# Performance work log

Hardware: AMD Instinct MI355X
Metric: run time of the kernel (lower is better)

## Reference

```python
import jax, jax.numpy as jnp
import numpy as np

B, G, T = 4096, 100, 24


def _greedy_dispatch(demand, caps, prices, slack_price):
    """Exact LP solution of: min prices@alloc + slack_price*slack
    s.t. 0<=alloc<=caps, sum(alloc)+slack = demand (per b,t).
    demand: [B,T] (nonneg), caps: [B,G,T], prices: [G], slack_price: scalar.
    Returns alloc [B,G,T], slack [B,T].
    """
    prices_all = jnp.concatenate([prices, slack_price[None]])        # [G+1]
    # slack capacity = demand itself (slack alone can absorb everything)
    caps_all = jnp.concatenate([caps, demand[:, None, :]], axis=1)    # [B,G+1,T]
    order = jnp.argsort(prices_all)                                   # merit order
    caps_s = caps_all[:, order, :]
    before = jnp.cumsum(caps_s, axis=1) - caps_s                      # capacity ahead in merit order
    alloc_s = jnp.clip(demand[:, None, :] - before, 0.0, caps_s)
    inv = jnp.argsort(order)
    alloc = alloc_s[:, inv, :]
    return alloc[:, :-1, :], alloc[:, -1, :]


def setup_inputs() -> dict:
    key = jax.random.key(0)
    k1, k2, k3, k4 = jax.random.split(key, 4)
    R_up = jax.random.uniform(k1, (B, G, T), dtype=jnp.float32)
    R_dn = jax.random.uniform(k2, (B, G, T), dtype=jnp.float32)
    omega_true = jax.random.normal(k3, (B, T), dtype=jnp.float32) * 5.0
    b_G = 10.0 + 40.0 * jax.random.uniform(k4, (G,), dtype=jnp.float32)  # marginal costs $/MWh
    return {
        "R_up": R_up,
        "R_dn": R_dn,
        "omega_true": omega_true,
        "b_G": b_G,
        "voll": jnp.float32(1000.0),
        "vosp": jnp.float32(500.0),
        "rt_up_ratio": jnp.float32(1.5),
        "rt_dn_ratio": jnp.float32(1.2),
    }


def reference(R_up, R_dn, omega_true, b_G, voll, vosp, rt_up_ratio, rt_dn_ratio):
    c_up = rt_up_ratio * b_G                                          # [G]
    c_dn = rt_dn_ratio * b_G                                          # [G]
    dem_up = jnp.maximum(omega_true, 0.0)                             # [B,T]
    dem_dn = jnp.maximum(-omega_true, 0.0)
    du, LS = _greedy_dispatch(dem_up, R_up, c_up, voll)
    dd, SP = _greedy_dispatch(dem_dn, R_dn, c_dn, vosp)
    rt_obj = (jnp.einsum('g,bgt->b', c_up, du)
              + jnp.einsum('g,bgt->b', c_dn, dd)
              + voll * LS.sum(axis=1) + vosp * SP.sum(axis=1))        # [B]
    return du, dd, LS, SP, rt_obj
```

## Files before the change

kernel.cpp:

```cpp
#include <hip/hip_runtime.h>

#define G_ 100
#define T_ 24
#define GP1 101
#define TILE (G_ * T_)
#define VPB (TILE / 4)
#define BLOCK 256
#define WPB 4

typedef float vfloat4 __attribute__((ext_vector_type(4)));

__global__ void setup_sort_kernel(const float* __restrict__ b_G,
                                  const float* __restrict__ voll,
                                  const float* __restrict__ vosp,
                                  const float* __restrict__ ru,
                                  const float* __restrict__ rd,
                                  int* __restrict__ order_out,
                                  float* __restrict__ price_out)
{
    __shared__ float pu[GP1], pd[GP1];
    int i = threadIdx.x;
    if (i < GP1) {
        if (i < G_) { float bg = b_G[i]; pu[i] = ru[0] * bg; pd[i] = rd[0] * bg; }
        else        { pu[i] = voll[0];   pd[i] = vosp[0]; }
    }
    __syncthreads();
    if (i < GP1) {
        float mu = pu[i], md = pd[i];
        int r0 = 0, r1 = 0;
        for (int j = 0; j < GP1; ++j) {
            float vu = pu[j], vd = pd[j];
            r0 += (vu < mu) || (vu == mu && j < i);
            r1 += (vd < md) || (vd == md && j < i);
        }
        order_out[r0] = i;        price_out[r0] = mu;
        order_out[GP1 + r1] = i;  price_out[GP1 + r1] = md;
    }
}

template<int N>
__device__ __forceinline__ void scan_chunk(int k0,
    float* __restrict__ tile, const int* __restrict__ ordp,
    const float* __restrict__ prp, float dem,
    float& before, float& objp, float& slackv)
{
    int gg[N]; float pr[N], cap[N];
#pragma unroll
    for (int j = 0; j < N; ++j) { gg[j] = ordp[k0 + j]; pr[j] = prp[k0 + j]; }
#pragma unroll
    for (int j = 0; j < N; ++j) {
        int gl = (gg[j] < G_) ? gg[j] : 0;
        cap[j] = tile[gl * T_];
    }
#pragma unroll
    for (int j = 0; j < N; ++j) {
        float c = (gg[j] == G_) ? dem : cap[j];
        float a = fminf(fmaxf(dem - before, 0.f), c);
        before += c;
        objp = fmaf(pr[j], a, objp);
        if (gg[j] == G_) slackv = a;
        else             tile[gg[j] * T_] = a;
    }
}

__global__ __launch_bounds__(BLOCK, 4) void dispatch_kernel(
    const float* __restrict__ R_up, const float* __restrict__ R_dn,
    const float* __restrict__ omega,
    const int* __restrict__ ord_ws, const float* __restrict__ pr_ws,
    float* __restrict__ out, int B)
{
    __shared__ float s_tile[WPB * TILE];
    __shared__ float s_obj[WPB];

    const int tid  = threadIdx.x;
    const int w    = tid >> 6;
    const int lane = tid & 63;
    const int b = __builtin_amdgcn_readfirstlane((blockIdx.x * WPB + w) >> 1);
    const int p = __builtin_amdgcn_readfirstlane(w & 1);

    const size_t bgt = (size_t)B * TILE;

    const vfloat4* __restrict__ src =
        (const vfloat4*)(p ? R_dn : R_up) + (size_t)b * VPB;
    vfloat4 buf[10];
#pragma unroll
    for (int j = 0; j < 9; ++j) buf[j] = src[lane + j * 64];
    if (lane < VPB - 576) buf[9] = src[lane + 576];

    float* __restrict__ tw = &s_tile[w * TILE];
#pragma unroll
    for (int j = 0; j < 9; ++j) *(vfloat4*)&tw[(lane + j * 64) * 4] = buf[j];
    if (lane < VPB - 576)       *(vfloat4*)&tw[(lane + 576) * 4]    = buf[9];
    __syncthreads();

    float objp = 0.f;
    if (lane < T_) {
        const float om  = omega[(size_t)b * T_ + lane];
        const float dem = p ? fmaxf(-om, 0.f) : fmaxf(om, 0.f);
        float* __restrict__ tile = tw + lane;
        const int*   __restrict__ ordp = ord_ws + p * GP1;
        const float* __restrict__ prp  = pr_ws  + p * GP1;
        float before = 0.f, slackv = 0.f;
        scan_chunk<16>( 0, tile, ordp, prp, dem, before, objp, slackv);
        scan_chunk<16>(16, tile, ordp, prp, dem, before, objp, slackv);
        scan_chunk<16>(32, tile, ordp, prp, dem, before, objp, slackv);
        scan_chunk<16>(48, tile, ordp, prp, dem, before, objp, slackv);
        scan_chunk<16>(64, tile, ordp, prp, dem, before, objp, slackv);
        scan_chunk<16>(80, tile, ordp, prp, dem, before, objp, slackv);
        scan_chunk< 5>(96, tile, ordp, prp, dem, before, objp, slackv);
        out[2 * bgt + (size_t)p * B * T_ + (size_t)b * T_ + lane] = slackv;
    }

#pragma unroll
    for (int off = 32; off; off >>= 1) objp += __shfl_xor(objp, off, 64);
    if (lane == 0) s_obj[w] = objp;
    __syncthreads();
    if (tid == 0)
        out[2 * bgt + 2 * (size_t)B * T_ + 2 * blockIdx.x]     = s_obj[0] + s_obj[1];
    if (tid == 64)
        out[2 * bgt + 2 * (size_t)B * T_ + 2 * blockIdx.x + 1] = s_obj[2] + s_obj[3];

    vfloat4* __restrict__ dst = (vfloat4*)out + ((size_t)p * B + b) * VPB;
#pragma unroll
    for (int j = 0; j < 9; ++j)
        dst[lane + j * 64] = *(const vfloat4*)&tw[(lane + j * 64) * 4];
    if (lane < VPB - 576)
        dst[lane + 576] = *(const vfloat4*)&tw[(lane + 576) * 4];
}

extern "C" void kernel_launch(void* const* d_in, const int* in_sizes, int n_in,
                              void* d_out, int out_size, void* d_ws, size_t ws_size,
                              hipStream_t stream)
{
    const float* R_up  = (const float*)d_in[0];
    const float* R_dn  = (const float*)d_in[1];
    const float* omega = (const float*)d_in[2];
    const float* b_G   = (const float*)d_in[3];
    const float* voll  = (const float*)d_in[4];
    const float* vosp  = (const float*)d_in[5];
    const float* ru    = (const float*)d_in[6];
    const float* rd    = (const float*)d_in[7];

    const int B = in_sizes[0] / TILE;
    float* out = (float*)d_out;

    int*   ord_ws = (int*)d_ws;
    float* pr_ws  = (float*)((char*)d_ws + 2 * GP1 * sizeof(int));

    setup_sort_kernel<<<1, 128, 0, stream>>>(b_G, voll, vosp, ru, rd, ord_ws, pr_ws);

    dispatch_kernel<<<(2 * B) / WPB, BLOCK, 0, stream>>>(
        R_up, R_dn, omega, ord_ws, pr_ws, out, B);
}
```

Measured before the change: 166.5 us.

## Process both up and down dispatch per wave with prefetch of down tile

Each wave now handles one batch element for both up and down directions instead of one direction, halving the grid. The R_dn tile is loaded into registers while the up scan runs, overlapping global loads with the LDS scan. Per-wave objective summation replaces the shared-memory cross-wave reduction and block-wide syncs, so only wave barriers remain. This halves the parallelism across waves and makes each wave's work serial across the two passes.

After: 172.5 us. 3.6% more time.

```diff
diff --git a/kernel.cpp b/kernel.cpp
--- a/kernel.cpp
+++ b/kernel.cpp
@@ -70,62 +70,74 @@
     float* __restrict__ out, int B)
 {
     __shared__ float s_tile[WPB * TILE];
-    __shared__ float s_obj[WPB];
 
     const int tid  = threadIdx.x;
     const int w    = tid >> 6;
     const int lane = tid & 63;
-    const int b = __builtin_amdgcn_readfirstlane((blockIdx.x * WPB + w) >> 1);
-    const int p = __builtin_amdgcn_readfirstlane(w & 1);
+    const int b    = __builtin_amdgcn_readfirstlane(blockIdx.x * WPB + w);
+    const size_t bgt = (size_t)B * TILE;
+    float* __restrict__ tw = &s_tile[w * TILE];
 
-    const size_t bgt = (size_t)B * TILE;
+    vfloat4 buf[10];
+    {
+        const vfloat4* __restrict__ s0 = (const vfloat4*)R_up + (size_t)b * VPB;
+#pragma unroll
+        for (int j = 0; j < 9; ++j) buf[j] = s0[lane + j * 64];
+        if (lane < VPB - 576) buf[9] = s0[lane + 576];
+    }
+    float om = 0.f;
+    if (lane < T_) om = omega[(size_t)b * T_ + lane];
 
-    const vfloat4* __restrict__ src =
-        (const vfloat4*)(p ? R_dn : R_up) + (size_t)b * VPB;
-    vfloat4 buf[10];
+    float objsum = 0.f;
 #pragma unroll
-    for (int j = 0; j < 9; ++j) buf[j] = src[lane + j * 64];
-    if (lane < VPB - 576) buf[9] = src[lane + 576];
+    for (int p = 0; p < 2; ++p) {
+#pragma unroll
+        for (int j = 0; j < 9; ++j) *(vfloat4*)&tw[(lane + j * 64) * 4] = buf[j];
+        if (lane < VPB - 576)       *(vfloat4*)&tw[(lane + 576) * 4]    = buf[9];
+        __builtin_amdgcn_wave_barrier();
 
-    float* __restrict__ tw = &s_tile[w * TILE];
+        if (p == 0) {
+            const vfloat4* __restrict__ s1 = (const vfloat4*)R_dn + (size_t)b * VPB;
 #pragma unroll
-    for (int j = 0; j < 9; ++j) *(vfloat4*)&tw[(lane + j * 64) * 4] = buf[j];
-    if (lane < VPB - 576)       *(vfloat4*)&tw[(lane + 576) * 4]    = buf[9];
-    __syncthreads();
+            for (int j = 0; j < 9; ++j) buf[j] = s1[lane + j * 64];
+            if (lane < VPB - 576) buf[9] = s1[lane + 576];
+        }
 
-    float objp = 0.f;
-    if (lane < T_) {
-        const float om  = omega[(size_t)b * T_ + lane];
-        const float dem = p ? fmaxf(-om, 0.f) : fmaxf(om, 0.f);
-        float* __restrict__ tile = tw + lane;
-        const int*   __restrict__ ordp = ord_ws + p * GP1;
-        const float* __restrict__ prp  = pr_ws  + p * GP1;
-        float before = 0.f, slackv = 0.f;
-        scan_chunk<16>( 0, tile, ordp, prp, dem, before, objp, slackv);
-        scan_chunk<16>(16, tile, ordp, prp, dem, before, objp, slackv);
-        scan_chunk<16>(32, tile, ordp, prp, dem, before, objp, slackv);
-        scan_chunk<16>(48, tile, ordp, prp, dem, before, objp, slackv);
-        scan_chunk<16>(64, tile, ordp, prp, dem, before, objp, slackv);
-        scan_chunk<16>(80, tile, ordp, prp, dem, before, objp, slackv);
-        scan_chunk< 5>(96, tile, ordp, prp, dem, before, objp, slackv);
-        out[2 * bgt + (size_t)p * B * T_ + (size_t)b * T_ + lane] = slackv;
+        float objp = 0.f;
+        if (lane < T_) {
+            const float dem = p ? fmaxf(-om, 0.f) : fmaxf(om, 0.f);
+            float* __restrict__ tile = tw + lane;
+            const int*   __restrict__ ordp = ord_ws + p * GP1;
+            const float* __restrict__ prp  = pr_ws  + p * GP1;
+            float before = 0.f, slackv = 0.f;
+            scan_chunk<16>( 0, tile, ordp, prp, dem, before, objp, slackv);
+            scan_chunk<16>(16, tile, ordp, prp, dem, before, objp, slackv);
+            scan_chunk<16>(32, tile, ordp, prp, dem, before, objp, slackv);
+            scan_chunk<16>(48, tile, ordp, prp, dem, before, objp, slackv);
+            scan_chunk<16>(64, tile, ordp, prp, dem, before, objp, slackv);
+            scan_chunk<16>(80, tile, ordp, prp, dem, before, objp, slackv);
+            scan_chunk< 5>(96, tile, ordp, prp, dem, before, objp, slackv);
+            out[2 * bgt + (size_t)p * B * T_ + (size_t)b * T_ + lane] = slackv;
+        }
+        __builtin_amdgcn_wave_barrier();
+
+#pragma unroll
+        for (int off = 32; off; off >>= 1) objp += __shfl_xor(objp, off, 64);
+        objsum += objp;
+
+        {
+            vfloat4* __restrict__ dst = (vfloat4*)out + ((size_t)p * B + b) * VPB;
+#pragma unroll
+            for (int j = 0; j < 9; ++j)
+                dst[lane + j * 64] = *(const vfloat4*)&tw[(lane + j * 64) * 4];
+            if (lane < VPB - 576)
+                dst[lane + 576] = *(const vfloat4*)&tw[(lane + 576) * 4];
+        }
+        __builtin_amdgcn_wave_barrier();
     }
 
-#pragma unroll
-    for (int off = 32; off; off >>= 1) objp += __shfl_xor(objp, off, 64);
-    if (lane == 0) s_obj[w] = objp;
-    __syncthreads();
-    if (tid == 0)
-        out[2 * bgt + 2 * (size_t)B * T_ + 2 * blockIdx.x]     = s_obj[0] + s_obj[1];
-    if (tid == 64)
-        out[2 * bgt + 2 * (size_t)B * T_ + 2 * blockIdx.x + 1] = s_obj[2] + s_obj[3];
-
-    vfloat4* __restrict__ dst = (vfloat4*)out + ((size_t)p * B + b) * VPB;
-#pragma unroll
-    for (int j = 0; j < 9; ++j)
-        dst[lane + j * 64] = *(const vfloat4*)&tw[(lane + j * 64) * 4];
-    if (lane < VPB - 576)
-        dst[lane + 576] = *(const vfloat4*)&tw[(lane + 576) * 4];
+    if (lane == 0)
+        out[2 * bgt + 2 * (size_t)B * T_ + b] = objsum;
 }
 
 extern "C" void kernel_launch(void* const* d_in, const int* in_sizes, int n_in,
@@ -149,6 +161,6 @@
 
     setup_sort_kernel<<<1, 128, 0, stream>>>(b_G, voll, vosp, ru, rd, ord_ws, pr_ws);
 
-    dispatch_kernel<<<(2 * B) / WPB, BLOCK, 0, stream>>>(
+    dispatch_kernel<<<B / WPB, BLOCK, 0, stream>>>(
         R_up, R_dn, omega, ord_ws, pr_ws, out, B);
 }
```

## Read capacities directly from global and stop the merit-order scan once demand is met

Applied to the files above, without the earlier changes.

The kernel no longer stages each full capacity tile into LDS. It zero-fills the LDS tile and reads only the capacities it needs, straight from global memory, in merit order. The scan runs in chunks of 8 and exits as soon as every lane's cumulative capacity covers its demand; the remaining allocations stay zero. Slack is computed after the loop as the leftover demand. This removes most of the input read traffic. In exchange it assumes the slack price sorts last (above every generator cost), and it trades coalesced vector loads for scattered dependent global reads.

Result: faster. 152.6 us (-8.4%).

```diff
diff --git a/kernel.cpp b/kernel.cpp
--- a/kernel.cpp
+++ b/kernel.cpp
@@ -5,8 +5,8 @@
 #define GP1 101
 #define TILE (G_ * T_)
 #define VPB (TILE / 4)
-#define BLOCK 256
 #define WPB 4
+#define BLOCK (64 * WPB)
 
 typedef float vfloat4 __attribute__((ext_vector_type(4)));
 
@@ -40,26 +40,22 @@
 
 template<int N>
 __device__ __forceinline__ void scan_chunk(int k0,
-    float* __restrict__ tile, const int* __restrict__ ordp,
-    const float* __restrict__ prp, float dem,
-    float& before, float& objp, float& slackv)
+    const float* __restrict__ capp,
+    const int* __restrict__ ordp, const float* __restrict__ prp,
+    float* __restrict__ ldscol,
+    float dem, float& before, float& objp)
 {
     int gg[N]; float pr[N], cap[N];
 #pragma unroll
     for (int j = 0; j < N; ++j) { gg[j] = ordp[k0 + j]; pr[j] = prp[k0 + j]; }
 #pragma unroll
-    for (int j = 0; j < N; ++j) {
-        int gl = (gg[j] < G_) ? gg[j] : 0;
-        cap[j] = tile[gl * T_];
-    }
+    for (int j = 0; j < N; ++j) cap[j] = capp[gg[j] * T_];
 #pragma unroll
     for (int j = 0; j < N; ++j) {
-        float c = (gg[j] == G_) ? dem : cap[j];
-        float a = fminf(fmaxf(dem - before, 0.f), c);
-        before += c;
+        float a = fminf(fmaxf(dem - before, 0.f), cap[j]);
+        before += cap[j];
         objp = fmaf(pr[j], a, objp);
-        if (gg[j] == G_) slackv = a;
-        else             tile[gg[j] * T_] = a;
+        ldscol[gg[j] * T_] = a;
     }
 }
 
@@ -75,57 +71,61 @@
     const int tid  = threadIdx.x;
     const int w    = tid >> 6;
     const int lane = tid & 63;
-    const int b = __builtin_amdgcn_readfirstlane((blockIdx.x * WPB + w) >> 1);
+    const int b = __builtin_amdgcn_readfirstlane(blockIdx.x * 2 + (w >> 1));
     const int p = __builtin_amdgcn_readfirstlane(w & 1);
+    const size_t bgt = (size_t)B * TILE;
+    float* __restrict__ tw = &s_tile[w * TILE];
 
-    const size_t bgt = (size_t)B * TILE;
+#pragma unroll
+    for (int j = 0; j < 9; ++j) *(vfloat4*)&tw[(lane + j * 64) * 4] = (vfloat4)(0.f);
+    if (lane < VPB - 576)       *(vfloat4*)&tw[(lane + 576) * 4]    = (vfloat4)(0.f);
 
-    const vfloat4* __restrict__ src =
-        (const vfloat4*)(p ? R_dn : R_up) + (size_t)b * VPB;
-    vfloat4 buf[10];
-#pragma unroll
-    for (int j = 0; j < 9; ++j) buf[j] = src[lane + j * 64];
-    if (lane < VPB - 576) buf[9] = src[lane + 576];
-
-    float* __restrict__ tw = &s_tile[w * TILE];
-#pragma unroll
-    for (int j = 0; j < 9; ++j) *(vfloat4*)&tw[(lane + j * 64) * 4] = buf[j];
-    if (lane < VPB - 576)       *(vfloat4*)&tw[(lane + 576) * 4]    = buf[9];
-    __syncthreads();
+    const int t = (lane < T_) ? lane : 0;
+    const int*   __restrict__ ordp = ord_ws + p * GP1;
+    const float* __restrict__ prp  = pr_ws  + p * GP1;
 
     float objp = 0.f;
     if (lane < T_) {
-        const float om  = omega[(size_t)b * T_ + lane];
+        const float om  = omega[(size_t)b * T_ + t];
         const float dem = p ? fmaxf(-om, 0.f) : fmaxf(om, 0.f);
-        float* __restrict__ tile = tw + lane;
-        const int*   __restrict__ ordp = ord_ws + p * GP1;
-        const float* __restrict__ prp  = pr_ws  + p * GP1;
-        float before = 0.f, slackv = 0.f;
-        scan_chunk<16>( 0, tile, ordp, prp, dem, before, objp, slackv);
-        scan_chunk<16>(16, tile, ordp, prp, dem, before, objp, slackv);
-        scan_chunk<16>(32, tile, ordp, prp, dem, before, objp, slackv);
-        scan_chunk<16>(48, tile, ordp, prp, dem, before, objp, slackv);
-        scan_chunk<16>(64, tile, ordp, prp, dem, before, objp, slackv);
-        scan_chunk<16>(80, tile, ordp, prp, dem, before, objp, slackv);
-        scan_chunk< 5>(96, tile, ordp, prp, dem, before, objp, slackv);
-        out[2 * bgt + (size_t)p * B * T_ + (size_t)b * T_ + lane] = slackv;
+        const float* __restrict__ capp = (p ? R_dn : R_up) + (size_t)b * TILE + t;
+        float* __restrict__ ldscol = tw + t;
+
+        float before = 0.f;
+        bool run = true;
+        int k = 0;
+        for (int c = 0; c < 12 && run; ++c) {
+            scan_chunk<8>(k, capp, ordp, prp, ldscol, dem, before, objp);
+            k += 8;
+            run = __any(before < dem);
+        }
+        if (run)
+            scan_chunk<4>(96, capp, ordp, prp, ldscol, dem, before, objp);
+
+        float slackv = fmaxf(dem - before, 0.f);
+        objp = fmaf(prp[GP1 - 1], slackv, objp);
+        out[2 * bgt + (size_t)p * B * T_ + (size_t)b * T_ + t] = slackv;
     }
 
 #pragma unroll
     for (int off = 32; off; off >>= 1) objp += __shfl_xor(objp, off, 64);
     if (lane == 0) s_obj[w] = objp;
+
+    __builtin_amdgcn_wave_barrier();
+    {
+        vfloat4* __restrict__ dst = (vfloat4*)out + ((size_t)p * B + b) * VPB;
+#pragma unroll
+        for (int j = 0; j < 9; ++j)
+            dst[lane + j * 64] = *(const vfloat4*)&tw[(lane + j * 64) * 4];
+        if (lane < VPB - 576)
+            dst[lane + 576] = *(const vfloat4*)&tw[(lane + 576) * 4];
+    }
+
     __syncthreads();
     if (tid == 0)
-        out[2 * bgt + 2 * (size_t)B * T_ + 2 * blockIdx.x]     = s_obj[0] + s_obj[1];
-    if (tid == 64)
-        out[2 * bgt + 2 * (size_t)B * T_ + 2 * blockIdx.x + 1] = s_obj[2] + s_obj[3];
-
-    vfloat4* __restrict__ dst = (vfloat4*)out + ((size_t)p * B + b) * VPB;
-#pragma unroll
-    for (int j = 0; j < 9; ++j)
-        dst[lane + j * 64] = *(const vfloat4*)&tw[(lane + j * 64) * 4];
-    if (lane < VPB - 576)
-        dst[lane + 576] = *(const vfloat4*)&tw[(lane + 576) * 4];
+        out[2 * bgt + 2 * (size_t)B * T_ + b]     = s_obj[0] + s_obj[1];
+    if (tid == 128)
+        out[2 * bgt + 2 * (size_t)B * T_ + b]     = s_obj[2] + s_obj[3];
 }
 
 extern "C" void kernel_launch(void* const* d_in, const int* in_sizes, int n_in,
@@ -149,6 +149,6 @@
 
     setup_sort_kernel<<<1, 128, 0, stream>>>(b_G, voll, vosp, ru, rd, ord_ws, pr_ws);
 
-    dispatch_kernel<<<(2 * B) / WPB, BLOCK, 0, stream>>>(
+    dispatch_kernel<<<B / 2, BLOCK, 0, stream>>>(
         R_up, R_dn, omega, ord_ws, pr_ws, out, B);
 }
```
